# Optimization experiments

Hardware: AMD Instinct MI355X
Metric: run time of the kernel (lower is better)

## Reference

```python
import jax, jax.numpy as jnp
import numpy as np

B = 2048; H = 300; L = 128; N = 131072


def _gru_dir(x, h0, w_ih, w_hh, b_ih, b_hh, reverse):
    # x: [B, L, H]; torch GRU gate order: r, z, n
    xp = jnp.einsum('blh,gh->blg', x, w_ih) + b_ih      # [B, L, 3H]
    xp = jnp.moveaxis(xp, 1, 0)                          # [L, B, 3H]

    def step(h, xp_t):
        xr, xz, xn = jnp.split(xp_t, 3, axis=-1)
        hp = h @ w_hh.T + b_hh
        hr, hz, hn = jnp.split(hp, 3, axis=-1)
        r = jax.nn.sigmoid(xr + hr)
        z = jax.nn.sigmoid(xz + hz)
        n = jnp.tanh(xn + r * hn)
        h_new = (1.0 - z) * n + z * h
        return h_new, h_new

    _, ys = jax.lax.scan(step, h0, xp, reverse=reverse)
    return jnp.moveaxis(ys, 0, 1)                        # [B, L, H]


def setup_inputs() -> dict:
    key = jax.random.key(0)
    ks = jax.random.split(key, 12)
    # ragged segment lengths: sum == N, max == L, min >= 1
    rng = np.random.default_rng(0)
    lengths = np.full(B, 64, dtype=np.int32)
    lengths[0] = 128; lengths[1] = 32; lengths[2] = 32
    d = rng.integers(0, 64, size=1022)
    lengths[4::2] = 64 + d
    lengths[5::2] = 64 - d
    assert lengths.sum() == N and lengths.max() == L and lengths.min() >= 1
    s = 1.0 / np.sqrt(H)
    u = lambda k, shape: jax.random.uniform(k, shape, jnp.float32, -s, s)
    return {
        'node': jax.random.normal(ks[0], (N, H), jnp.float32),
        'a_scope': jnp.asarray(lengths, jnp.int32),
        'max_len': L,
        'bias': u(ks[1], (H,)),
        'w_ih_f': u(ks[2], (3 * H, H)),
        'w_hh_f': u(ks[3], (3 * H, H)),
        'b_ih_f': u(ks[4], (3 * H,)),
        'b_hh_f': u(ks[5], (3 * H,)),
        'w_ih_b': u(ks[6], (3 * H, H)),
        'w_hh_b': u(ks[7], (3 * H, H)),
        'b_ih_b': u(ks[8], (3 * H,)),
        'b_hh_b': u(ks[9], (3 * H,)),
    }


def reference(node, a_scope, max_len, bias, w_ih_f, w_hh_f, b_ih_f, b_hh_f,
              w_ih_b, w_hh_b, b_ih_b, b_hh_b):
    n_total = node.shape[0]
    message = jax.nn.relu(node + bias)
    ends = jnp.cumsum(a_scope)
    starts = ends - a_scope
    pos = jnp.arange(max_len)
    idx = jnp.clip(starts[:, None] + pos[None, :], 0, n_total - 1)   # [B, L]
    valid = pos[None, :] < a_scope[:, None]                          # [B, L]
    # initial hidden: per-segment max of raw node features
    gathered = node[idx]                                             # [B, L, H]
    h0 = jnp.max(jnp.where(valid[..., None], gathered, -jnp.inf), axis=1)  # [B, H]
    # zero-padded messages (padding rows ARE processed by the GRU, as in torch)
    msg_pad = jnp.where(valid[..., None], message[idx], 0.0)         # [B, L, H]
    out_f = _gru_dir(msg_pad, h0, w_ih_f, w_hh_f, b_ih_f, b_hh_f, reverse=False)
    out_b = _gru_dir(msg_pad, h0, w_ih_b, w_hh_b, b_ih_b, b_hh_b, reverse=True)
    out = jnp.concatenate([out_f, out_b], axis=-1)                   # [B, L, 2H]
    # unpad back to flat ragged layout [N, 2H]
    n_idx = jnp.arange(n_total)
    b_idx = jnp.searchsorted(ends, n_idx, side='right')
    l_idx = n_idx - starts[b_idx]
    return out[b_idx, l_idx]
```

## Files before the change

### kernel.cpp

```cpp
#include <hip/hip_runtime.h>
#include <cstddef>
#include <cstdint>


typedef short s8v __attribute__((ext_vector_type(8)));
typedef float f4v __attribute__((ext_vector_type(4)));

#define NSEG   2048
#define HID    300
#define HPAD   320
#define MAXLEN 128
#define NTOT   131072
#define PKSTRIDE 307200

__device__ __forceinline__ short f2bf(float f){
  unsigned u = __float_as_uint(f);
  u = (u + 0x7FFFu + ((u >> 16) & 1u)) >> 16;
  return (short)u;
}
__device__ __forceinline__ float bf2f(unsigned short u){
  return __uint_as_float((unsigned)u << 16);
}
__device__ __forceinline__ float sigm(float x){ return 1.f / (1.f + __expf(-x)); }
__device__ __forceinline__ float tanha(float x){ return 1.f - 2.f / (__expf(2.f * x) + 1.f); }

__global__ __launch_bounds__(1024)
void scan_starts_k(const int* __restrict__ a_scope, int* __restrict__ starts){
  __shared__ int buf[2][NSEG];
  const int tid = threadIdx.x;
  for (int i = tid; i < NSEG; i += 1024) buf[0][i] = a_scope[i];
  __syncthreads();
  int src = 0;
  for (int off = 1; off < NSEG; off <<= 1){
    for (int i = tid; i < NSEG; i += 1024){
      int v = buf[src][i];
      if (i >= off) v += buf[src][i - off];
      buf[1 - src][i] = v;
    }
    __syncthreads();
    src ^= 1;
  }
  for (int i = tid; i < NSEG; i += 1024) starts[i] = buf[src][i] - a_scope[i];
}

__global__ void h0_max_k(const float* __restrict__ node, const int* __restrict__ a_scope,
                         const int* __restrict__ starts, float* __restrict__ h0){
  const int b = blockIdx.x;
  const int k = threadIdx.x;
  const int s = starts[b], len = a_scope[b];
  float m = 0.f;
  if (k < HID){
    m = -3.402823466e38f;
    const float* p = node + (size_t)s * HID + k;
    for (int t = 0; t < len; ++t) m = fmaxf(m, p[(size_t)t * HID]);
  }
  h0[(size_t)b * HPAD + k] = m;
}

__global__ __launch_bounds__(256)
void sort_segs_k(const int* __restrict__ a_scope, int* __restrict__ perm,
                 int* __restrict__ gmax){
  __shared__ int cnt[MAXLEN + 1];
  __shared__ int sp[NSEG];
  const int tid = threadIdx.x;
  for (int i = tid; i < MAXLEN + 1; i += 256) cnt[i] = 0;
  __syncthreads();
  for (int i = tid; i < NSEG; i += 256) atomicAdd(&cnt[MAXLEN - a_scope[i]], 1);
  __syncthreads();
  if (tid == 0){
    int s = 0;
    for (int b = 0; b <= MAXLEN; ++b){ int c = cnt[b]; cnt[b] = s; s += c; }
  }
  __syncthreads();
  for (int i = tid; i < NSEG; i += 256){
    int p = atomicAdd(&cnt[MAXLEN - a_scope[i]], 1);
    sp[p] = i;
  }
  __syncthreads();
  for (int i = tid; i < NSEG; i += 256) perm[i] = sp[i];
  for (int g = tid; g < NSEG / 16; g += 256) gmax[g] = a_scope[sp[g * 16]];
}

__global__ void prep2_k(const float* __restrict__ wih_f, const float* __restrict__ whh_f,
                        const float* __restrict__ bih_f, const float* __restrict__ bhh_f,
                        const float* __restrict__ wih_b, const float* __restrict__ whh_b,
                        const float* __restrict__ bih_b, const float* __restrict__ bhh_b,
                        short* __restrict__ PkH, short* __restrict__ PkI,
                        float* __restrict__ gbias){
  const int idx = blockIdx.x * 256 + threadIdx.x;
  if (idx < 1228800){
    const bool isH = idx < 614400;
    int t = isH ? idx : idx - 614400;
    int e = t & 7, lane = (t >> 3) & 63;
    int r = t >> 9;
    int kt = r % 10; r /= 10;
    int jt = r % 20; r /= 20;
    int sec = r % 3, d = r / 3;
    const float* w = isH ? (d ? whh_b : whh_f) : (d ? wih_b : wih_f);
    int j = jt * 16 + (lane & 15);
    int k = kt * 32 + (lane >> 4) * 8 + e;
    float v = 0.f;
    if (j < HID && k < HID) v = w[(sec * HID + j) * HID + k];
    (isH ? PkH : PkI)[t] = f2bf(v);
  } else if (idx < 1228800 + 2560){
    int r3 = idx - 1228800;
    int d = r3 / 1280;
    int rem = r3 - d * 1280;
    int sec = rem / HPAD;
    int j = rem - sec * HPAD;
    const float* bih = d ? bih_b : bih_f;
    const float* bhh = d ? bhh_b : bhh_f;
    float v = 0.f;
    if (j < HID){
      if (sec == 0)      v = bih[j] + bhh[j];
      else if (sec == 1) v = bih[HID + j] + bhh[HID + j];
      else if (sec == 2) v = bih[2 * HID + j];
      else               v = bhh[2 * HID + j];
    }
    gbias[r3] = v;
  }
}

__global__ __launch_bounds__(256)
void xp_gemm_k(const float* __restrict__ node, const float* __restrict__ bias,
               const short* __restrict__ PkI, short* __restrict__ xp){
  __shared__ __align__(16) short Bt[4 * 5120];
  const int dir = blockIdx.x & 1;
  const int blk = blockIdx.x >> 1;
  const int tid = threadIdx.x;
  const int wave = tid >> 6, lane = tid & 63;
  const int quad = lane >> 4, lc = lane & 15, l8 = lane << 3;
  const int rowbase = blk * 128 + wave * 32;
  const short* PI = PkI + (size_t)dir * PKSTRIDE;
  short* xpd = xp + (size_t)dir * ((size_t)NTOT * 900);

  s8v A[2][10];
  #pragma unroll
  for (int tm = 0; tm < 2; ++tm){
    const float* src = node + (size_t)(rowbase + tm * 16 + lc) * HID;
    #pragma unroll
    for (int kt = 0; kt < 10; ++kt){
      const int k0 = kt * 32 + quad * 8;
      s8v a;
      #pragma unroll
      for (int e = 0; e < 8; ++e){
        const int k = k0 + e;
        float v = 0.f;
        if (k < HID){ v = src[k] + bias[k]; v = v > 0.f ? v : 0.f; }
        a[e] = f2bf(v);
      }
      A[tm][kt] = a;
    }
  }

  for (int st0 = 0; st0 < 60; st0 += 4){
    __syncthreads();
    for (int i = tid; i < 2560; i += 256)
      ((s8v*)Bt)[i] = ((const s8v*)(PI + (size_t)st0 * 5120))[i];
    __syncthreads();
    #pragma unroll
    for (int u = 0; u < 4; ++u){
      const int st = st0 + u;
      const int sec = st / 20, jt = st % 20;
      f4v a0 = {0.f,0.f,0.f,0.f}, a1 = {0.f,0.f,0.f,0.f};
      #pragma unroll
      for (int kt = 0; kt < 10; ++kt){
        const s8v b = *(const s8v*)&Bt[u * 5120 + kt * 512 + l8];
        a0 = __builtin_amdgcn_mfma_f32_16x16x32_bf16(A[0][kt], b, a0, 0, 0, 0);
        a1 = __builtin_amdgcn_mfma_f32_16x16x32_bf16(A[1][kt], b, a1, 0, 0, 0);
      }
      const int j = jt * 16 + lc;
      if (j < HID){
        const int g = sec * HID + j;
        #pragma unroll
        for (int r = 0; r < 4; ++r){
          const int rr = rowbase + quad * 4 + r;
          xpd[(size_t)rr * 900 + g]        = f2bf(a0[r]);
          xpd[(size_t)(rr + 16) * 900 + g] = f2bf(a1[r]);
        }
      }
    }
  }
}

__global__ __launch_bounds__(640)
void gru5_k(const int* __restrict__ a_scope, const int* __restrict__ starts,
            const int* __restrict__ perm, const int* __restrict__ gmax,
            const float* __restrict__ h0, const short* __restrict__ PkH,
            const float* __restrict__ gbias, const short* __restrict__ xp,
            float* __restrict__ out){
  __shared__ __align__(16) short WL[114 * 512];
  __shared__ __align__(16) short hbuf[16][328];
  __shared__ __align__(16) short xbuf[16][908];
  __shared__ int lsL[16], llL[16];

  const int dir  = blockIdx.x & 1;
  const int g    = blockIdx.x >> 1;
  const int seg0 = g * 16;
  const int tid  = threadIdx.x;
  const int wave = tid >> 6;
  const int lane = tid & 63;
  const int quad = lane >> 4;
  const int lc   = lane & 15;
  const int l8   = lane << 3;
  const int jt0  = 2 * wave;
  const int njt  = (jt0 < 18) ? 2 : 1;

  const short* PH = PkH + (size_t)dir * PKSTRIDE;

  s8v Bp[2][3][2];
  #pragma unroll
  for (int i = 0; i < 2; ++i)
    #pragma unroll
    for (int s = 0; s < 3; ++s)
      #pragma unroll
      for (int ktp = 0; ktp < 2; ++ktp)
        Bp[i][s][ktp] = *(const s8v*)(PH + (size_t)((s * 20 + jt0 + i) * 10 + 2 + ktp) * 512 + l8);

  #pragma unroll
  for (int i = 0; i < 2; ++i){
    if (i < njt){
      #pragma unroll
      for (int s = 0; s < 3; ++s)
        #pragma unroll
        for (int ktl = 0; ktl < 2; ++ktl)
          *(s8v*)&WL[(size_t)(wave * 12 + (i * 3 + s) * 2 + ktl) * 512 + l8] =
            *(const s8v*)(PH + (size_t)((s * 20 + jt0 + i) * 10 + ktl) * 512 + l8);
    }
  }

  if (tid < 16){
    const int sg = perm[seg0 + tid];
    lsL[tid] = starts[sg];
    llL[tid] = a_scope[sg];
  }

  for (int i = tid; i < 16 * HPAD; i += 640){
    const int m = i / HPAD, k = i - m * HPAD;
    hbuf[m][k] = f2bf(h0[(size_t)perm[seg0 + m] * HPAD + k]);
  }

  float hprev[2][4];
  float bR[2], bZ[2], bX[2], bH[2];
  bool  jv[2];
  #pragma unroll
  for (int i = 0; i < 2; ++i){
    const int jt = jt0 + i;
    const int j  = jt * 16 + lc;
    jv[i] = (jt < 19) && (j < HID);
    bR[i] = bZ[i] = bX[i] = bH[i] = 0.f;
    hprev[i][0] = hprev[i][1] = hprev[i][2] = hprev[i][3] = 0.f;
    if (jv[i]){
      bR[i] = gbias[dir * 1280 + 0 * HPAD + j];
      bZ[i] = gbias[dir * 1280 + 1 * HPAD + j];
      bX[i] = gbias[dir * 1280 + 2 * HPAD + j];
      bH[i] = gbias[dir * 1280 + 3 * HPAD + j];
      #pragma unroll
      for (int r = 0; r < 4; ++r)
        hprev[i][r] = h0[(size_t)perm[seg0 + quad * 4 + r] * HPAD + j];
    }
  }
  __syncthreads();

  int ls_r[4], ll_r[4];
  #pragma unroll
  for (int r = 0; r < 4; ++r){
    ls_r[r] = lsL[quad * 4 + r];
    ll_r[r] = llL[quad * 4 + r];
  }
  const int sm_ = tid / 40;
  const int su_ = tid - sm_ * 40;
  const int myls = lsL[sm_], myll = llL[sm_];

  const unsigned short* xpd = (const unsigned short*)xp + (size_t)dir * ((size_t)NTOT * 900);
  const int nsteps = dir ? MAXLEN : gmax[g];

  for (int step = 0; step < nsteps; ++step){
    const int t = dir ? (MAXLEN - 1 - step) : step;

    {
      const bool sv = t < myll;
      const unsigned short* sp_ = xpd + (size_t)(myls + t) * 900;
      for (int u = su_; u < 225; u += 40){
        unsigned long long v = 0ull;
        if (sv) v = *(const unsigned long long*)(sp_ + u * 4);
        *(unsigned long long*)&xbuf[sm_][u * 4] = v;
      }
    }

    __syncthreads();

    f4v acc[2][3];
    #pragma unroll
    for (int i = 0; i < 2; ++i)
      #pragma unroll
      for (int s = 0; s < 3; ++s)
        acc[i][s] = f4v{0.f, 0.f, 0.f, 0.f};

    #pragma unroll
    for (int ktl = 0; ktl < 2; ++ktl){
      const s8v a = *(const s8v*)&hbuf[lc][ktl * 32 + quad * 8];
      #pragma unroll
      for (int i = 0; i < 2; ++i){
        if (i < njt){
          #pragma unroll
          for (int s = 0; s < 3; ++s){
            const s8v b = *(const s8v*)&WL[(size_t)(wave * 12 + (i * 3 + s) * 2 + ktl) * 512 + l8];
            acc[i][s] = __builtin_amdgcn_mfma_f32_16x16x32_bf16(a, b, acc[i][s], 0, 0, 0);
          }
        }
      }
    }
    #pragma unroll
    for (int ktp = 0; ktp < 2; ++ktp){
      const s8v a = *(const s8v*)&hbuf[lc][(2 + ktp) * 32 + quad * 8];
      #pragma unroll
      for (int i = 0; i < 2; ++i)
        #pragma unroll
        for (int s = 0; s < 3; ++s)
          acc[i][s] = __builtin_amdgcn_mfma_f32_16x16x32_bf16(a, Bp[i][s][ktp], acc[i][s], 0, 0, 0);
    }
    #pragma unroll 2
    for (int kt = 4; kt < 10; ++kt){
      const s8v a = *(const s8v*)&hbuf[lc][kt * 32 + quad * 8];
      #pragma unroll
      for (int i = 0; i < 2; ++i)
        #pragma unroll
        for (int s = 0; s < 3; ++s){
          const s8v b = *(const s8v*)(PH + (size_t)((s * 20 + jt0 + i) * 10 + kt) * 512 + l8);
          acc[i][s] = __builtin_amdgcn_mfma_f32_16x16x32_bf16(a, b, acc[i][s], 0, 0, 0);
        }
    }

    float xg[2][4][3];
    #pragma unroll
    for (int i = 0; i < 2; ++i){
      const int j = (jt0 + i) * 16 + lc;
      #pragma unroll
      for (int r = 0; r < 4; ++r){
        const int m = quad * 4 + r;
        float vr = 0.f, vz = 0.f, vn = 0.f;
        if (jv[i]){
          vr = bf2f((unsigned short)xbuf[m][j]);
          vz = bf2f((unsigned short)xbuf[m][j + 300]);
          vn = bf2f((unsigned short)xbuf[m][j + 600]);
        }
        xg[i][r][0] = vr; xg[i][r][1] = vz; xg[i][r][2] = vn;
      }
    }

    __syncthreads();

    #pragma unroll
    for (int i = 0; i < 2; ++i){
      if (jv[i]){
        const int j = (jt0 + i) * 16 + lc;
        #pragma unroll
        for (int r = 0; r < 4; ++r){
          const int m = quad * 4 + r;
          const float rg = sigm(acc[i][0][r] + bR[i] + xg[i][r][0]);
          const float zg = sigm(acc[i][1][r] + bZ[i] + xg[i][r][1]);
          const float ng = tanha(xg[i][r][2] + bX[i] + rg * (acc[i][2][r] + bH[i]));
          const float hnew = (1.f - zg) * ng + zg * hprev[i][r];
          hprev[i][r] = hnew;
          hbuf[m][j] = f2bf(hnew);
          if (t < ll_r[r])
            out[(size_t)(ls_r[r] + t) * 600 + dir * HID + j] = hnew;
        }
      }
    }
  }
}

__global__ void prep_k(const float* __restrict__ wih_f, const float* __restrict__ whh_f,
                       const float* __restrict__ bih_f, const float* __restrict__ bhh_f,
                       const float* __restrict__ wih_b, const float* __restrict__ whh_b,
                       const float* __restrict__ bih_b, const float* __restrict__ bhh_b,
                       short* __restrict__ PkA, short* __restrict__ PkB,
                       float* __restrict__ gbias){
  const int idx = blockIdx.x * 256 + threadIdx.x;
  if (idx < 819200){
    int e = idx & 7, lane = (idx >> 3) & 63;
    int r = idx >> 9;
    int kt = r % 20; r /= 20;
    int jt = r % 20; r /= 20;
    int sec = r & 1, d = r >> 1;
    const float* wih = d ? wih_b : wih_f;
    const float* whh = d ? whh_b : whh_f;
    int j = jt * 16 + (lane & 15);
    int k = kt * 32 + (lane >> 4) * 8 + e;
    float v = 0.f;
    if (j < HID){
      int row = sec * HID + j;
      if (k < HID)                    v = wih[row * HID + k];
      else if (k >= 320 && k < 620)   v = whh[row * HID + (k - 320)];
    }
    PkA[idx] = f2bf(v);
  } else if (idx < 819200 + 409600){
    int t = idx - 819200;
    int e = t & 7, lane = (t >> 3) & 63;
    int r = t >> 9;
    int kt = r % 10; r /= 10;
    int jt = r % 20; r /= 20;
    int sec = r & 1, d = r >> 1;
    const float* w = sec ? (d ? whh_b : whh_f) : (d ? wih_b : wih_f);
    int j = jt * 16 + (lane & 15);
    int k = kt * 32 + (lane >> 4) * 8 + e;
    float v = 0.f;
    if (j < HID && k < HID) v = w[(600 + j) * HID + k];
    PkB[t] = f2bf(v);
  } else if (idx < 819200 + 409600 + 2560){
    int r3 = idx - 819200 - 409600;
    int d = r3 / 1280;
    int rem = r3 - d * 1280;
    int sec = rem / HPAD;
    int j = rem - sec * HPAD;
    const float* bih = d ? bih_b : bih_f;
    const float* bhh = d ? bhh_b : bhh_f;
    float v = 0.f;
    if (j < HID){
      if (sec == 0)      v = bih[j] + bhh[j];
      else if (sec == 1) v = bih[HID + j] + bhh[HID + j];
      else if (sec == 2) v = bih[2 * HID + j];
      else               v = bhh[2 * HID + j];
    }
    gbias[r3] = v;
  }
}

__global__ __launch_bounds__(256)
void gru_k(const float* __restrict__ node, const float* __restrict__ bias,
           const int* __restrict__ a_scope, const int* __restrict__ starts,
           const float* __restrict__ h0, const short* __restrict__ PkA,
           const short* __restrict__ PkB, const float* __restrict__ gbias,
           float* __restrict__ out){
  __shared__ __align__(16) short xbuf[16][328];
  __shared__ __align__(16) short hbuf[16][328];
  __shared__ float hfp[16][324];
  __shared__ float lbias[4][HPAD];
  __shared__ int ls[16], ll[16];

  const int dir  = blockIdx.x & 1;
  const int seg0 = (blockIdx.x >> 1) * 16;
  const int tid  = threadIdx.x;
  const int wave = tid >> 6;
  const int lane = tid & 63;
  const int quad = lane >> 4;
  const int lc   = lane & 15;
  const int l8   = lane << 3;

  if (tid < 16){ ls[tid] = starts[seg0 + tid]; ll[tid] = a_scope[seg0 + tid]; }
  for (int i = tid; i < 4 * HPAD; i += 256) ((float*)lbias)[i] = gbias[dir * (4 * HPAD) + i];
  for (int i = tid; i < 16 * HPAD; i += 256){
    int m = i / HPAD, k = i - m * HPAD;
    float v = h0[(size_t)(seg0 + m) * HPAD + k];
    hfp[m][k] = v;
    hbuf[m][k] = f2bf(v);
  }
  __syncthreads();

  const short* PA = PkA + (size_t)dir * 409600;
  const short* PB = PkB + (size_t)dir * 204800;
  const int xm = tid >> 4, xu = tid & 15;

  for (int step = 0; step < MAXLEN; ++step){
    const int t = dir ? (MAXLEN - 1 - step) : step;
    {
      const bool valid = t < ll[xm];
      const float* src = node + (size_t)(ls[xm] + t) * HID;
      for (int k = xu; k < HPAD; k += 16){
        float v = 0.f;
        if (valid && k < HID){
          v = src[k] + bias[k];
          v = v > 0.f ? v : 0.f;
        }
        xbuf[xm][k] = f2bf(v);
      }
    }
    __syncthreads();

    f4v aR[5], aZ[5], aX[5], aH[5];
    #pragma unroll
    for (int i = 0; i < 5; ++i){
      aR[i] = f4v{0.f,0.f,0.f,0.f}; aZ[i] = f4v{0.f,0.f,0.f,0.f};
      aX[i] = f4v{0.f,0.f,0.f,0.f}; aH[i] = f4v{0.f,0.f,0.f,0.f};
    }
    #pragma unroll 2
    for (int kt = 0; kt < 10; ++kt){
      const int k0 = kt * 32 + quad * 8;
      const s8v a = *(const s8v*)&xbuf[lc][k0];
      #pragma unroll
      for (int i = 0; i < 5; ++i){
        const int jt = wave * 5 + i;
        const s8v bR = *(const s8v*)(PA + (size_t)((jt)      * 20 + kt) * 512 + l8);
        aR[i] = __builtin_amdgcn_mfma_f32_16x16x32_bf16(a, bR, aR[i], 0, 0, 0);
        const s8v bZ = *(const s8v*)(PA + (size_t)((20 + jt) * 20 + kt) * 512 + l8);
        aZ[i] = __builtin_amdgcn_mfma_f32_16x16x32_bf16(a, bZ, aZ[i], 0, 0, 0);
        const s8v bX = *(const s8v*)(PB + (size_t)((jt)      * 10 + kt) * 512 + l8);
        aX[i] = __builtin_amdgcn_mfma_f32_16x16x32_bf16(a, bX, aX[i], 0, 0, 0);
      }
    }
    #pragma unroll 2
    for (int kt = 0; kt < 10; ++kt){
      const int k0 = kt * 32 + quad * 8;
      const s8v a = *(const s8v*)&hbuf[lc][k0];
      #pragma unroll
      for (int i = 0; i < 5; ++i){
        const int jt = wave * 5 + i;
        const s8v bR = *(const s8v*)(PA + (size_t)((jt)      * 20 + 10 + kt) * 512 + l8);
        aR[i] = __builtin_amdgcn_mfma_f32_16x16x32_bf16(a, bR, aR[i], 0, 0, 0);
        const s8v bZ = *(const s8v*)(PA + (size_t)((20 + jt) * 20 + 10 + kt) * 512 + l8);
        aZ[i] = __builtin_amdgcn_mfma_f32_16x16x32_bf16(a, bZ, aZ[i], 0, 0, 0);
        const s8v bH = *(const s8v*)(PB + (size_t)((20 + jt) * 10 + kt) * 512 + l8);
        aH[i] = __builtin_amdgcn_mfma_f32_16x16x32_bf16(a, bH, aH[i], 0, 0, 0);
      }
    }
    __syncthreads();

    #pragma unroll
    for (int i = 0; i < 5; ++i){
      const int j = wave * 80 + i * 16 + lc;
      if (j < HID){
        const float bR = lbias[0][j], bZ = lbias[1][j];
        const float bX = lbias[2][j], bH = lbias[3][j];
        #pragma unroll
        for (int r = 0; r < 4; ++r){
          const int m = quad * 4 + r;
          const float rg = sigm(aR[i][r] + bR);
          const float zg = sigm(aZ[i][r] + bZ);
          const float ng = tanha(aX[i][r] + bX + rg * (aH[i][r] + bH));
          const float hold = hfp[m][j];
          const float hnew = (1.f - zg) * ng + zg * hold;
          hfp[m][j] = hnew;
          hbuf[m][j] = f2bf(hnew);
          if (t < ll[m])
            out[(size_t)(ls[m] + t) * 600 + dir * HID + j] = hnew;
        }
      }
    }
  }
}

extern "C" void kernel_launch(void* const* d_in, const int* in_sizes, int n_in,
                              void* d_out, int out_size, void* d_ws, size_t ws_size,
                              hipStream_t stream){
  const float* node    = (const float*)d_in[0];
  const int*   a_scope = (const int*)  d_in[1];
  const float* bias    = (const float*)d_in[3];
  const float* wih_f   = (const float*)d_in[4];
  const float* whh_f   = (const float*)d_in[5];
  const float* bih_f   = (const float*)d_in[6];
  const float* bhh_f   = (const float*)d_in[7];
  const float* wih_b   = (const float*)d_in[8];
  const float* whh_b   = (const float*)d_in[9];
  const float* bih_b   = (const float*)d_in[10];
  const float* bhh_b   = (const float*)d_in[11];
  float* out = (float*)d_out;

  char* ws = (char*)d_ws;
  int*   starts = (int*)  (ws + 0);
  float* h0     = (float*)(ws + 8192);

  scan_starts_k<<<1, 1024, 0, stream>>>(a_scope, starts);
  h0_max_k<<<NSEG, HPAD, 0, stream>>>(node, a_scope, starts, h0);

  const size_t FAST_NEED = 476956672ull;
  if (ws_size >= FAST_NEED){
    short* PkH = (short*)(ws + 2629632);
    short* PkI = (short*)(ws + 3858432);
    float* gb  = (float*)(ws + 5087232);
    short* xpb = (short*)(ws + 5097472);
    int* perm = (int*)(ws + 3858432);
    int* gmx  = (int*)(ws + 3858432 + 8192);
    prep2_k<<<4810, 256, 0, stream>>>(wih_f, whh_f, bih_f, bhh_f,
                                      wih_b, whh_b, bih_b, bhh_b, PkH, PkI, gb);
    xp_gemm_k<<<2048, 256, 0, stream>>>(node, bias, PkI, xpb);
    sort_segs_k<<<1, 256, 0, stream>>>(a_scope, perm, gmx);
    gru5_k<<<256, 640, 0, stream>>>(a_scope, starts, perm, gmx, h0, PkH, gb, xpb, out);
  } else {
    short* PkA   = (short*)(ws + 2629632);
    short* PkB   = (short*)(ws + 4268032);
    float* gbias = (float*)(ws + 5087232);
    prep_k<<<4810, 256, 0, stream>>>(wih_f, whh_f, bih_f, bhh_f,
                                     wih_b, whh_b, bih_b, bhh_b, PkA, PkB, gbias);
    gru_k<<<256, 256, 0, stream>>>(node, bias, a_scope, starts, h0, PkA, PkB, gbias, out);
  }
}
```

Baseline: 2.196 ms.

## Double-buffer hidden state and prefetch input projections into registers per step

Replaces the shared-memory staging of the per-step input projection with direct per-lane register loads that are prefetched one step ahead. Double-buffers the hidden-state tile in LDS so each step needs one barrier instead of two. Drops the register-cached weight slices and streams those k-tiles from global memory instead. The aim is to cut per-step synchronization and take the xp staging off the recurrence critical path, at the cost of scattered 2-byte global loads and more global weight traffic.

```diff
diff --git a/kernel.cpp b/kernel.cpp
--- a/kernel.cpp
+++ b/kernel.cpp
@@ -184,14 +184,13 @@
 }
 
 __global__ __launch_bounds__(640)
-void gru5_k(const int* __restrict__ a_scope, const int* __restrict__ starts,
+void gru6_k(const int* __restrict__ a_scope, const int* __restrict__ starts,
             const int* __restrict__ perm, const int* __restrict__ gmax,
             const float* __restrict__ h0, const short* __restrict__ PkH,
             const float* __restrict__ gbias, const short* __restrict__ xp,
             float* __restrict__ out){
-  __shared__ __align__(16) short WL[114 * 512];
-  __shared__ __align__(16) short hbuf[16][328];
-  __shared__ __align__(16) short xbuf[16][908];
+  __shared__ __align__(16) short WL[120 * 512];
+  __shared__ __align__(16) short hbuf[2][16][328];
   __shared__ int lsL[16], llL[16];
 
   const int dir  = blockIdx.x & 1;
@@ -204,30 +203,17 @@
   const int lc   = lane & 15;
   const int l8   = lane << 3;
   const int jt0  = 2 * wave;
-  const int njt  = (jt0 < 18) ? 2 : 1;
 
   const short* PH = PkH + (size_t)dir * PKSTRIDE;
 
-  s8v Bp[2][3][2];
   #pragma unroll
   for (int i = 0; i < 2; ++i)
     #pragma unroll
     for (int s = 0; s < 3; ++s)
       #pragma unroll
-      for (int ktp = 0; ktp < 2; ++ktp)
-        Bp[i][s][ktp] = *(const s8v*)(PH + (size_t)((s * 20 + jt0 + i) * 10 + 2 + ktp) * 512 + l8);
-
-  #pragma unroll
-  for (int i = 0; i < 2; ++i){
-    if (i < njt){
-      #pragma unroll
-      for (int s = 0; s < 3; ++s)
-        #pragma unroll
-        for (int ktl = 0; ktl < 2; ++ktl)
-          *(s8v*)&WL[(size_t)(wave * 12 + (i * 3 + s) * 2 + ktl) * 512 + l8] =
-            *(const s8v*)(PH + (size_t)((s * 20 + jt0 + i) * 10 + ktl) * 512 + l8);
-    }
-  }
+      for (int ktl = 0; ktl < 2; ++ktl)
+        *(s8v*)&WL[(size_t)(wave * 12 + (i * 3 + s) * 2 + ktl) * 512 + l8] =
+          *(const s8v*)(PH + (size_t)((s * 20 + jt0 + i) * 10 + ktl) * 512 + l8);
 
   if (tid < 16){
     const int sg = perm[seg0 + tid];
@@ -237,7 +223,8 @@
 
   for (int i = tid; i < 16 * HPAD; i += 640){
     const int m = i / HPAD, k = i - m * HPAD;
-    hbuf[m][k] = f2bf(h0[(size_t)perm[seg0 + m] * HPAD + k]);
+    hbuf[0][m][k] = f2bf(h0[(size_t)perm[seg0 + m] * HPAD + k]);
+    hbuf[1][m][k] = 0;
   }
 
   float hprev[2][4];
@@ -268,28 +255,29 @@
     ls_r[r] = lsL[quad * 4 + r];
     ll_r[r] = llL[quad * 4 + r];
   }
-  const int sm_ = tid / 40;
-  const int su_ = tid - sm_ * 40;
-  const int myls = lsL[sm_], myll = llL[sm_];
 
   const unsigned short* xpd = (const unsigned short*)xp + (size_t)dir * ((size_t)NTOT * 900);
   const int nsteps = dir ? MAXLEN : gmax[g];
 
+  unsigned short xgr[2][4][3];
+  {
+    const int t0 = dir ? (MAXLEN - 1) : 0;
+    #pragma unroll
+    for (int r = 0; r < 4; ++r){
+      int idx = ls_r[r] + t0; if (idx > NTOT - 1) idx = NTOT - 1;
+      const unsigned short* p = xpd + (size_t)idx * 900;
+      #pragma unroll
+      for (int i = 0; i < 2; ++i){
+        const unsigned short* pj = p + (jv[i] ? ((jt0 + i) * 16 + lc) : 0);
+        xgr[i][r][0] = pj[0]; xgr[i][r][1] = pj[300]; xgr[i][r][2] = pj[600];
+      }
+    }
+  }
+
+  int cur = 0;
   for (int step = 0; step < nsteps; ++step){
     const int t = dir ? (MAXLEN - 1 - step) : step;
 
-    {
-      const bool sv = t < myll;
-      const unsigned short* sp_ = xpd + (size_t)(myls + t) * 900;
-      for (int u = su_; u < 225; u += 40){
-        unsigned long long v = 0ull;
-        if (sv) v = *(const unsigned long long*)(sp_ + u * 4);
-        *(unsigned long long*)&xbuf[sm_][u * 4] = v;
-      }
-    }
-
-    __syncthreads();
-
     f4v acc[2][3];
     #pragma unroll
     for (int i = 0; i < 2; ++i)
@@ -299,30 +287,18 @@
 
     #pragma unroll
     for (int ktl = 0; ktl < 2; ++ktl){
-      const s8v a = *(const s8v*)&hbuf[lc][ktl * 32 + quad * 8];
-      #pragma unroll
-      for (int i = 0; i < 2; ++i){
-        if (i < njt){
-          #pragma unroll
-          for (int s = 0; s < 3; ++s){
-            const s8v b = *(const s8v*)&WL[(size_t)(wave * 12 + (i * 3 + s) * 2 + ktl) * 512 + l8];
-            acc[i][s] = __builtin_amdgcn_mfma_f32_16x16x32_bf16(a, b, acc[i][s], 0, 0, 0);
-          }
-        }
-      }
-    }
-    #pragma unroll
-    for (int ktp = 0; ktp < 2; ++ktp){
-      const s8v a = *(const s8v*)&hbuf[lc][(2 + ktp) * 32 + quad * 8];
+      const s8v a = *(const s8v*)&hbuf[cur][lc][ktl * 32 + quad * 8];
       #pragma unroll
       for (int i = 0; i < 2; ++i)
         #pragma unroll
-        for (int s = 0; s < 3; ++s)
-          acc[i][s] = __builtin_amdgcn_mfma_f32_16x16x32_bf16(a, Bp[i][s][ktp], acc[i][s], 0, 0, 0);
-    }
-    #pragma unroll 2
-    for (int kt = 4; kt < 10; ++kt){
-      const s8v a = *(const s8v*)&hbuf[lc][kt * 32 + quad * 8];
+        for (int s = 0; s < 3; ++s){
+          const s8v b = *(const s8v*)&WL[(size_t)(wave * 12 + (i * 3 + s) * 2 + ktl) * 512 + l8];
+          acc[i][s] = __builtin_amdgcn_mfma_f32_16x16x32_bf16(a, b, acc[i][s], 0, 0, 0);
+        }
+    }
+    #pragma unroll 4
+    for (int kt = 2; kt < 10; ++kt){
+      const s8v a = *(const s8v*)&hbuf[cur][lc][kt * 32 + quad * 8];
       #pragma unroll
       for (int i = 0; i < 2; ++i)
         #pragma unroll
@@ -331,25 +307,6 @@
           acc[i][s] = __builtin_amdgcn_mfma_f32_16x16x32_bf16(a, b, acc[i][s], 0, 0, 0);
         }
     }
-
-    float xg[2][4][3];
-    #pragma unroll
-    for (int i = 0; i < 2; ++i){
-      const int j = (jt0 + i) * 16 + lc;
-      #pragma unroll
-      for (int r = 0; r < 4; ++r){
-        const int m = quad * 4 + r;
-        float vr = 0.f, vz = 0.f, vn = 0.f;
-        if (jv[i]){
-          vr = bf2f((unsigned short)xbuf[m][j]);
-          vz = bf2f((unsigned short)xbuf[m][j + 300]);
-          vn = bf2f((unsigned short)xbuf[m][j + 600]);
-        }
-        xg[i][r][0] = vr; xg[i][r][1] = vz; xg[i][r][2] = vn;
-      }
-    }
-
-    __syncthreads();
 
     #pragma unroll
     for (int i = 0; i < 2; ++i){
@@ -358,17 +315,39 @@
         #pragma unroll
         for (int r = 0; r < 4; ++r){
           const int m = quad * 4 + r;
-          const float rg = sigm(acc[i][0][r] + bR[i] + xg[i][r][0]);
-          const float zg = sigm(acc[i][1][r] + bZ[i] + xg[i][r][1]);
-          const float ng = tanha(xg[i][r][2] + bX[i] + rg * (acc[i][2][r] + bH[i]));
+          const bool v = t < ll_r[r];
+          const float xr = v ? bf2f(xgr[i][r][0]) : 0.f;
+          const float xz = v ? bf2f(xgr[i][r][1]) : 0.f;
+          const float xn = v ? bf2f(xgr[i][r][2]) : 0.f;
+          const float rg = sigm(acc[i][0][r] + bR[i] + xr);
+          const float zg = sigm(acc[i][1][r] + bZ[i] + xz);
+          const float ng = tanha(xn + bX[i] + rg * (acc[i][2][r] + bH[i]));
           const float hnew = (1.f - zg) * ng + zg * hprev[i][r];
           hprev[i][r] = hnew;
-          hbuf[m][j] = f2bf(hnew);
-          if (t < ll_r[r])
-            out[(size_t)(ls_r[r] + t) * 600 + dir * HID + j] = hnew;
-        }
-      }
-    }
+          hbuf[cur ^ 1][m][j] = f2bf(hnew);
+          if (v) out[(size_t)(ls_r[r] + t) * 600 + dir * HID + j] = hnew;
+        }
+      }
+    }
+
+    {
+      int tn = dir ? (t - 1) : (t + 1);
+      if (tn < 0) tn = 0;
+      if (tn > MAXLEN - 1) tn = MAXLEN - 1;
+      #pragma unroll
+      for (int r = 0; r < 4; ++r){
+        int idx = ls_r[r] + tn; if (idx > NTOT - 1) idx = NTOT - 1;
+        const unsigned short* p = xpd + (size_t)idx * 900;
+        #pragma unroll
+        for (int i = 0; i < 2; ++i){
+          const unsigned short* pj = p + (jv[i] ? ((jt0 + i) * 16 + lc) : 0);
+          xgr[i][r][0] = pj[0]; xgr[i][r][1] = pj[300]; xgr[i][r][2] = pj[600];
+        }
+      }
+    }
+
+    asm volatile("s_waitcnt lgkmcnt(0)\n\ts_barrier" ::: "memory");
+    cur ^= 1;
   }
 }
 
@@ -576,7 +555,7 @@
                                       wih_b, whh_b, bih_b, bhh_b, PkH, PkI, gb);
     xp_gemm_k<<<2048, 256, 0, stream>>>(node, bias, PkI, xpb);
     sort_segs_k<<<1, 256, 0, stream>>>(a_scope, perm, gmx);
-    gru5_k<<<256, 640, 0, stream>>>(a_scope, starts, perm, gmx, h0, PkH, gb, xpb, out);
+    gru6_k<<<256, 640, 0, stream>>>(a_scope, starts, perm, gmx, h0, PkH, gb, xpb, out);
   } else {
     short* PkA   = (short*)(ws + 2629632);
     short* PkB   = (short*)(ws + 4268032);
```

Measured after the change: 1.868 ms. 14.9% less time.
